# Performance work log

Hardware: AMD Instinct MI355X
Metric: run time of the kernel (lower is better)

Reference implementation:

```python
import jax, jax.numpy as jnp
import numpy as np

B, C_IN, T = 32, 22, 5000
EMB, P = 64, 100
HOP, NFFT, SR = 25, 128, 250
MIN_SZ, MAX_SZ = 10, 100
OC = 40
SCALES = (9, 25, 49)
FC = OC * len(SCALES)
_freqs = np.arange(NFFT // 2 + 1) * SR / NFFT
MU_IDX = np.nonzero((_freqs >= 8) & (_freqs <= 13))[0]   # bins 5,6
BETA_IDX = np.nonzero((_freqs >= 13) & (_freqs <= 30))[0]  # bins 7..15


def setup_inputs() -> dict:
    key = jax.random.key(0)
    k = iter(jax.random.split(key, 16))
    inp = {"x": jax.random.normal(next(k), (B, C_IN, T), jnp.float32)}
    for i, s in enumerate(SCALES):
        inp[f"ms{i}_w1"] = jax.random.normal(next(k), (OC, 1, 1, s), jnp.float32) * 0.05
        inp[f"ms{i}_b1"] = jnp.zeros((OC,), jnp.float32)
        inp[f"ms{i}_w2"] = jax.random.normal(next(k), (OC, OC, C_IN, 1), jnp.float32) * 0.05
        inp[f"ms{i}_b2"] = jnp.zeros((OC,), jnp.float32)
        inp[f"ms{i}_g"] = jnp.ones((OC,), jnp.float32)
        inp[f"ms{i}_bt"] = jnp.zeros((OC,), jnp.float32)
        inp[f"ms{i}_m"] = jnp.zeros((OC,), jnp.float32)
        inp[f"ms{i}_v"] = jnp.ones((OC,), jnp.float32)
    inp["a_w1"] = jax.random.normal(next(k), (C_IN // 2, C_IN, 3), jnp.float32) * 0.05
    inp["a_b1"] = jnp.zeros((C_IN // 2,), jnp.float32)
    inp["a_g"] = jnp.ones((C_IN // 2,), jnp.float32)
    inp["a_bt"] = jnp.zeros((C_IN // 2,), jnp.float32)
    inp["a_m"] = jnp.zeros((C_IN // 2,), jnp.float32)
    inp["a_v"] = jnp.ones((C_IN // 2,), jnp.float32)
    inp["a_w2"] = jax.random.normal(next(k), (1, C_IN // 2, 1), jnp.float32) * 0.05
    inp["a_b2"] = jnp.zeros((1,), jnp.float32)
    inp["proj_w"] = jax.random.normal(next(k), (EMB, FC, 1), jnp.float32) * 0.05
    inp["proj_b"] = jnp.zeros((EMB,), jnp.float32)
    return inp


def _conv1d(x, w, pad):
    return jax.lax.conv_general_dilated(x, w, (1,), [(pad, pad)],
                                        dimension_numbers=("NCH", "OIH", "NCH"))


def _bn(y, g, bt, m, v):  # eval-mode BatchNorm over channel dim of [B, C, T]
    return (y - m[None, :, None]) * jax.lax.rsqrt(v[None, :, None] + 1e-5) * g[None, :, None] + bt[None, :, None]


def _branch(x, w1, b1, w2, b2, g, bt, m, v):
    # Conv2d(1,OC,(1,ks)) on [B,1,C,T] == per-channel 1D conv over time.
    oc, _, _, ks = w1.shape
    b_, c_, t_ = x.shape
    y = _conv1d(x.reshape(b_ * c_, 1, t_), w1.reshape(oc, 1, ks), (ks - 1) // 2) + b1[None, :, None]
    y = y.reshape(b_, c_, oc, t_).transpose(0, 2, 1, 3)            # [B, OC, C, T]
    # Conv2d(OC,OC,(C,1)) collapses the channel (height) dim.
    y = jnp.einsum("oih,biht->bot", w2[..., 0], y) + b2[None, :, None]
    return jax.nn.elu(_bn(y, g, bt, m, v))                         # [B, OC, T]


def _stft_power(x):
    # torchaudio Spectrogram: center=True, reflect pad, periodic hann, power=2
    pad = NFFT // 2
    xp = jnp.pad(x, ((0, 0), (0, 0), (pad, pad)), mode="reflect")
    nfr = T // HOP  # module truncates to t // hop frames
    idx = jnp.arange(nfr)[:, None] * HOP + jnp.arange(NFFT)[None, :]
    win = 0.5 * (1.0 - jnp.cos(2.0 * jnp.pi * jnp.arange(NFFT) / NFFT))
    frames = xp[..., idx] * win                                    # [B, C, nfr, NFFT]
    spec = jnp.fft.rfft(frames, axis=-1)
    return spec.real ** 2 + spec.imag ** 2                         # [B, C, nfr, NFFT//2+1]


def _interp_linear(a, n):  # F.interpolate(mode='linear', align_corners=False) on [B, L]
    L = a.shape[-1]
    pos = jnp.clip((jnp.arange(n) + 0.5) * (L / n) - 0.5, 0.0, L - 1.0)
    lo = jnp.floor(pos).astype(jnp.int32)
    hi = jnp.minimum(lo + 1, L - 1)
    w = pos - lo
    return a[:, lo] * (1.0 - w) + a[:, hi] * w


def _adaptive_grid(act):
    w = 1.0 / (act + 1e-6)
    w = w / jnp.sum(w, axis=1, keepdims=True)
    gs = jnp.clip(w * T, MIN_SZ, MAX_SZ)
    gs = gs * (T / jnp.sum(gs, axis=1, keepdims=True))
    gsr = jnp.round(gs).astype(jnp.int32)
    gsr = gsr.at[:, -1].add(T - jnp.sum(gsr, axis=1))
    gsf = jnp.clip(gsr, MIN_SZ, MAX_SZ)
    gsf = gsf.at[:, -1].add(T - jnp.sum(gsf, axis=1))
    return jnp.where(gsf < MIN_SZ, MIN_SZ, gsf)


def _forward(x, ms0_w1, ms0_b1, ms0_w2, ms0_b2, ms0_g, ms0_bt, ms0_m, ms0_v,
             ms1_w1, ms1_b1, ms1_w2, ms1_b2, ms1_g, ms1_bt, ms1_m, ms1_v,
             ms2_w1, ms2_b1, ms2_w2, ms2_b2, ms2_g, ms2_bt, ms2_m, ms2_v,
             a_w1, a_b1, a_g, a_bt, a_m, a_v, a_w2, a_b2, proj_w, proj_b):
    # ---- frequency-domain activity detector ----
    spec = _stft_power(x)                                          # [B, C, 200, F]
    comb = spec[..., MU_IDX].mean(-1) + spec[..., BETA_IDX].mean(-1)  # [B, C, 200]
    a = jax.nn.relu(_bn(_conv1d(comb, a_w1, 1) + a_b1[None, :, None], a_g, a_bt, a_m, a_v))
    a = jnp.einsum("oi,bit->bot", a_w2[..., 0], a)[:, 0] + a_b2[0]
    activity = jax.nn.sigmoid(a)                                   # [B, 200]
    act_i = _interp_linear(activity, P)                            # [B, P]
    grid = _adaptive_grid(act_i)                                   # [B, P] int32, sums ~= T
    ends = jnp.cumsum(grid, axis=1)
    starts = ends - grid
    # ---- multi-scale CNN features ----
    feats = jnp.concatenate([
        _branch(x, ms0_w1, ms0_b1, ms0_w2, ms0_b2, ms0_g, ms0_bt, ms0_m, ms0_v),
        _branch(x, ms1_w1, ms1_b1, ms1_w2, ms1_b2, ms1_g, ms1_bt, ms1_m, ms1_v),
        _branch(x, ms2_w1, ms2_b1, ms2_w2, ms2_b2, ms2_g, ms2_bt, ms2_m, ms2_v)],
        axis=1)                                                    # [B, FC, T]
    # ---- ragged per-patch avg+max pooling via segment reductions ----
    tix = jnp.arange(T)
    seg = jax.vmap(lambda e: jnp.searchsorted(e, tix, side="right"))(ends)  # [B,T] in [0,P]
    flat = (seg + jnp.arange(B)[:, None] * (P + 1)).reshape(-1)
    f = feats.transpose(0, 2, 1).reshape(B * T, FC)
    nseg = B * (P + 1)  # extra slot collects any overflow timesteps
    sums = jax.ops.segment_sum(f, flat, num_segments=nseg)
    cnt = jax.ops.segment_sum(jnp.ones((B * T, 1), f.dtype), flat, num_segments=nseg)
    mx = jax.ops.segment_max(f, flat, num_segments=nseg)
    avg = sums / jnp.maximum(cnt, 1.0)
    mx = jnp.where(cnt > 0, mx, 0.0)
    pooled = (avg + mx).reshape(B, P + 1, FC)[:, :P]               # combined avg+max
    valid = ((ends <= T) & (starts < ends))[..., None]
    pooled = jnp.where(valid, pooled, 0.0)
    emb = jnp.einsum("oc,bpc->bpo", proj_w[..., 0], pooled) + proj_b  # [B, P, EMB]
    return emb, grid, act_i


def reference(x, ms0_w1, ms0_b1, ms0_w2, ms0_b2, ms0_g, ms0_bt, ms0_m, ms0_v,
              ms1_w1, ms1_b1, ms1_w2, ms1_b2, ms1_g, ms1_bt, ms1_m, ms1_v,
              ms2_w1, ms2_b1, ms2_w2, ms2_b2, ms2_g, ms2_bt, ms2_m, ms2_v,
              a_w1, a_b1, a_g, a_bt, a_m, a_v, a_w2, a_b2, proj_w, proj_b):
    return _forward(x, ms0_w1, ms0_b1, ms0_w2, ms0_b2, ms0_g, ms0_bt, ms0_m, ms0_v,
                    ms1_w1, ms1_b1, ms1_w2, ms1_b2, ms1_g, ms1_bt, ms1_m, ms1_v,
                    ms2_w1, ms2_b1, ms2_w2, ms2_b2, ms2_g, ms2_bt, ms2_m, ms2_v,
                    a_w1, a_b1, a_g, a_bt, a_m, a_v, a_w2, a_b2, proj_w, proj_b)
```

## Files before the change

kernel.cpp:

```cpp
#include <hip/hip_runtime.h>
#include <hip/hip_bf16.h>
#include <hip/hip_fp8.h>
#include <math.h>
#include <string.h>

#define B 32
#define CIN 22
#define T 5000
#define EMB 64
#define P 100
#define HOP 25
#define OC 40
#define FC 120
#define NBIN 11
#define NFR 200

#define TCH 256
#define CROWS 304
#define RS8 40

#define XPAD 5128
#define TWROW 24

typedef __attribute__((ext_vector_type(4))) float f32x4;

__device__ __forceinline__ unsigned short f2bf(float f) {
  unsigned u = __float_as_uint(f);
  unsigned r = (u + 0x7FFFu + ((u >> 16) & 1u)) >> 16;
  return (unsigned short)r;
}
__device__ __forceinline__ float bf2f(unsigned short u) {
  return __uint_as_float(((unsigned)u) << 16);
}
__device__ __forceinline__ unsigned char f2fp8(float f) {
  __hip_fp8_e4m3 q(f);
  return (unsigned char)q.__x;
}
__device__ __forceinline__ float fast_elu(float y) {
  return y > 0.f ? y : (__builtin_amdgcn_exp2f(y * 1.44269504088896340736f) - 1.0f);
}
__device__ __forceinline__ unsigned pack2bf(float a, float b) {
  __hip_bfloat162 h = __float22bfloat162_rn(make_float2(a, b));
  unsigned u;
  memcpy(&u, &h, 4);
  return u;
}
__device__ __forceinline__ float wave_sum_f(float v) {
  #pragma unroll
  for (int off = 1; off < 64; off <<= 1) v += __shfl_xor(v, off);
  return v;
}
__device__ __forceinline__ int wave_sum_i(int v) {
  #pragma unroll
  for (int off = 1; off < 64; off <<= 1) v += __shfl_xor(v, off);
  return v;
}

struct SetupArgs {
  const float* w1[3]; const float* b1[3]; const float* w2[3]; const float* b2[3];
  const float* g[3];  const float* bt[3]; const float* m[3];  const float* v[3];
  unsigned char* pw8;
  float* A; float* Bc; float* tw;
};

__global__ __launch_bounds__(256) void setup_all(SetupArgs args) {
  int bx = blockIdx.x;
  int tid = threadIdx.x;
  if (bx < 498) {
    int id = bx * 256 + tid;
    int s, KS, fbase, idl;
    if (id < 13824)       { s = 0; KS = 9;  fbase = 0;   idl = id; }
    else if (id < 52224)  { s = 1; KS = 25; fbase = 27;  idl = id - 13824; }
    else                  { s = 2; KS = 49; fbase = 102; idl = id - 52224; }
    int fi = idl >> 9, rem = idl & 511;
    int lane = rem >> 3, j = rem & 7;
    int k = fi / 3, ot = fi - k * 3;
    int m = lane & 15, h = ((lane >> 4) << 3) + j;
    int o = ot * 16 + m;
    float val = 0.f;
    if (h < CIN && o < OC) {
      const float* w1 = args.w1[s];
      const float* w2 = args.w2[s];
      for (int i = 0; i < OC; ++i)
        val = fmaf(w2[(o * OC + i) * CIN + h], w1[i * KS + k], val);
    }
    args.pw8[(size_t)(fbase + fi) * 512 + rem] = f2fp8(val);
  } else if (bx < 504) {
    int id = (bx - 498) * 256 + tid;
    if (id < 1408) {
      int n = id & 127, k = id >> 7;
      const double PI = 3.14159265358979323846;
      double ang = -2.0 * PI * (double)((k + 5) * n) / 128.0;
      double win = 0.5 * (1.0 - cos(2.0 * PI * (double)n / 128.0));
      args.tw[n * TWROW + 2 * k]     = (float)(cos(ang) * win);
      args.tw[n * TWROW + 2 * k + 1] = (float)(sin(ang) * win);
    } else if (id < 1536) {
      int n = id - 1408;
      args.tw[n * TWROW + 22] = 0.f;
      args.tw[n * TWROW + 23] = 0.f;
    }
  } else {
    if (tid < 120) {
      int s = tid / 40, o = tid - s * 40;
      const float* w2 = args.w2[s];
      float sc = args.g[s][o] / sqrtf(args.v[s][o] + 1e-5f);
      float cc = args.b2[s][o];
      for (int i = 0; i < OC; ++i) {
        float sh = 0.f;
        for (int h = 0; h < CIN; ++h) sh += w2[(o * OC + i) * CIN + h];
        cc = fmaf(args.b1[s][i], sh, cc);
      }
      args.A[tid] = sc;
      args.Bc[tid] = cc * sc + (args.bt[s][o] - args.m[s][o] * sc);
    }
  }
}

__global__ __launch_bounds__(256) void stft_comb(const float* __restrict__ x,
                                                 const float* __restrict__ tw,
                                                 float* __restrict__ comb) {
  __shared__ float xsh[XPAD];
  int bc = blockIdx.x;
  const float* xr = x + (size_t)bc * T;
  int tid = threadIdx.x;
  for (int i = tid; i < XPAD; i += 256) {
    int mm = i - 64;
    mm = (mm < 0) ? -mm : mm;
    mm = (mm >= T) ? (2 * T - 2 - mm) : mm;
    xsh[i] = xr[mm];
  }
  __syncthreads();
  int fr = tid;
  if (fr < NFR) {
    float cr[NBIN], ci[NBIN];
    #pragma unroll
    for (int k = 0; k < NBIN; ++k) { cr[k] = 0.f; ci[k] = 0.f; }
    const float* xw = xsh + fr * HOP;
    #pragma unroll 2
    for (int n = 0; n < 128; ++n) {
      float xv = xw[n];
      const float4* t4 = reinterpret_cast<const float4*>(tw + n * TWROW);
      float4 w0 = t4[0], w1 = t4[1], w2 = t4[2], w3 = t4[3], w4 = t4[4], w5 = t4[5];
      cr[0] = fmaf(xv, w0.x, cr[0]); ci[0] = fmaf(xv, w0.y, ci[0]);
      cr[1] = fmaf(xv, w0.z, cr[1]); ci[1] = fmaf(xv, w0.w, ci[1]);
      cr[2] = fmaf(xv, w1.x, cr[2]); ci[2] = fmaf(xv, w1.y, ci[2]);
      cr[3] = fmaf(xv, w1.z, cr[3]); ci[3] = fmaf(xv, w1.w, ci[3]);
      cr[4] = fmaf(xv, w2.x, cr[4]); ci[4] = fmaf(xv, w2.y, ci[4]);
      cr[5] = fmaf(xv, w2.z, cr[5]); ci[5] = fmaf(xv, w2.w, ci[5]);
      cr[6] = fmaf(xv, w3.x, cr[6]); ci[6] = fmaf(xv, w3.y, ci[6]);
      cr[7] = fmaf(xv, w3.z, cr[7]); ci[7] = fmaf(xv, w3.w, ci[7]);
      cr[8] = fmaf(xv, w4.x, cr[8]); ci[8] = fmaf(xv, w4.y, ci[8]);
      cr[9] = fmaf(xv, w4.z, cr[9]); ci[9] = fmaf(xv, w4.w, ci[9]);
      cr[10] = fmaf(xv, w5.x, cr[10]); ci[10] = fmaf(xv, w5.y, ci[10]);
    }
    float p[NBIN];
    #pragma unroll
    for (int k = 0; k < NBIN; ++k) p[k] = cr[k] * cr[k] + ci[k] * ci[k];
    float beta = 0.f;
    #pragma unroll
    for (int k = 2; k < NBIN; ++k) beta += p[k];
    comb[bc * NFR + fr] = 0.5f * (p[0] + p[1]) + beta * (1.f / 9.f);
  }
}

struct MidSmem {
  union {
    struct {
      float cl[CIN * NFR];
      float actL[NFR];
      float aiL[P];
      float fL[P];
      int giL[P];
      int sI[P];
      float red;
    } a;
    unsigned char xs8[CROWS * RS8];
  };
};

template <int KS, int FB, int SBASE>
__device__ __forceinline__ void scale_body(const unsigned char* __restrict__ xs8,
                                           const unsigned char* __restrict__ pw8,
                                           const float* __restrict__ Aff,
                                           const float* __restrict__ Bff,
                                           unsigned short* __restrict__ feats,
                                           int b, int t0, int wt0, int lane) {
  constexpr int PAD = (KS - 1) / 2;
  const int n = lane & 15, q = lane >> 4;
  f32x4 acc[3][4];
  #pragma unroll
  for (int ot = 0; ot < 3; ++ot)
    #pragma unroll
    for (int ti = 0; ti < 4; ++ti)
      acc[ot][ti] = (f32x4){0.f, 0.f, 0.f, 0.f};

  const unsigned char* pws = pw8 + (size_t)FB * 512 + lane * 8;
  long long A0 = *(const long long*)(pws);
  long long A1 = *(const long long*)(pws + 512);
  long long A2 = *(const long long*)(pws + 1024);
  #pragma unroll 1
  for (int k = 0; k < KS; ++k) {
    long long nA0 = 0, nA1 = 0, nA2 = 0;
    if (k + 1 < KS) {
      const unsigned char* p = pws + (size_t)(k + 1) * 3 * 512;
      nA0 = *(const long long*)(p);
      nA1 = *(const long long*)(p + 512);
      nA2 = *(const long long*)(p + 1024);
    }
    int rbase = 24 - PAD + k + wt0 + n;
    #pragma unroll
    for (int ti = 0; ti < 4; ++ti) {
      long long Bf = *(const long long*)(xs8 + (rbase + ti * 16) * RS8 + q * 8);
      acc[0][ti] = __builtin_amdgcn_mfma_f32_16x16x32_fp8_fp8(A0, Bf, acc[0][ti], 0, 0, 0);
      acc[1][ti] = __builtin_amdgcn_mfma_f32_16x16x32_fp8_fp8(A1, Bf, acc[1][ti], 0, 0, 0);
      acc[2][ti] = __builtin_amdgcn_mfma_f32_16x16x32_fp8_fp8(A2, Bf, acc[2][ti], 0, 0, 0);
    }
    A0 = nA0; A1 = nA1; A2 = nA2;
  }
  #pragma unroll
  for (int ot = 0; ot < 3; ++ot) {
    int obase = ot * 16 + q * 4;
    if (obase < OC) {
      float Av0 = Aff[SBASE + obase + 0], Bv0 = Bff[SBASE + obase + 0];
      float Av1 = Aff[SBASE + obase + 1], Bv1 = Bff[SBASE + obase + 1];
      float Av2 = Aff[SBASE + obase + 2], Bv2 = Bff[SBASE + obase + 2];
      float Av3 = Aff[SBASE + obase + 3], Bv3 = Bff[SBASE + obase + 3];
      #pragma unroll
      for (int ti = 0; ti < 4; ++ti) {
        int tt = t0 + wt0 + ti * 16 + n;
        if (tt < T) {
          uint2 pk;
          pk.x = pack2bf(fast_elu(fmaf(acc[ot][ti][0], Av0, Bv0)),
                         fast_elu(fmaf(acc[ot][ti][1], Av1, Bv1)));
          pk.y = pack2bf(fast_elu(fmaf(acc[ot][ti][2], Av2, Bv2)),
                         fast_elu(fmaf(acc[ot][ti][3], Av3, Bv3)));
          *reinterpret_cast<uint2*>(feats + (size_t)(b * T + tt) * FC + SBASE + obase) = pk;
        }
      }
    }
  }
}

struct MidArgs {
  const float* x;
  const unsigned char* pw8;
  const float* Aff; const float* Bff;
  unsigned short* feats;
  const float* comb;
  const float* aw1; const float* ab1;
  const float* ag;  const float* abt;
  const float* am;  const float* av;
  const float* aw2; const float* ab2;
  float* out_grid; float* out_acti;
  int* ends_i; int* grid_i;
};

__global__ __launch_bounds__(256) void mid_all(MidArgs args) {
  __shared__ MidSmem sm;
  int bx = blockIdx.x;
  int tid = threadIdx.x;
  if (bx >= B) {
    int cx = bx - B;
    int s = cx % 3;
    int rem = cx / 3;
    int b = rem / 20, t0 = (rem - b * 20) * TCH;
    for (int i = tid; i < CROWS * RS8 / 4; i += 256)
      reinterpret_cast<unsigned*>(sm.xs8)[i] = 0u;
    __syncthreads();
    for (int idx = tid; idx < CIN * CROWS; idx += 256) {
      int h = idx / CROWS, tl = idx - h * CROWS;
      int gt = t0 - 24 + tl;
      float v = (gt >= 0 && gt < T) ? args.x[(size_t)(b * CIN + h) * T + gt] : 0.f;
      sm.xs8[tl * RS8 + h] = f2fp8(v);
    }
    __syncthreads();
    int wv = tid >> 6, lane = tid & 63;
    int wt0 = wv * 64;
    if (s == 0)
      scale_body<9, 0, 0>(sm.xs8, args.pw8, args.Aff, args.Bff, args.feats, b, t0, wt0, lane);
    else if (s == 1)
      scale_body<25, 27, 40>(sm.xs8, args.pw8, args.Aff, args.Bff, args.feats, b, t0, wt0, lane);
    else
      scale_body<49, 102, 80>(sm.xs8, args.pw8, args.Aff, args.Bff, args.feats, b, t0, wt0, lane);
  } else {
    int b = bx;
    for (int i = tid; i < CIN * NFR; i += 256) sm.a.cl[i] = args.comb[b * CIN * NFR + i];
    __syncthreads();
    int t = tid;
    if (t < NFR) {
      float z = args.ab2[0];
      for (int o = 0; o < 11; ++o) {
        float s = args.ab1[o];
        for (int i = 0; i < CIN; ++i) {
          const float* wr = args.aw1 + o * 66 + i * 3;
          const float* crow = sm.a.cl + i * NFR;
          if (t > 0)       s = fmaf(wr[0], crow[t - 1], s);
          s = fmaf(wr[1], crow[t], s);
          if (t < NFR - 1) s = fmaf(wr[2], crow[t + 1], s);
        }
        float rs = 1.0f / sqrtf(args.av[o] + 1e-5f);
        float y = (s - args.am[o]) * rs * args.ag[o] + args.abt[o];
        y = fmaxf(y, 0.f);
        z = fmaf(args.aw2[o], y, z);
      }
      sm.a.actL[t] = 1.f / (1.f + expf(-z));
    }
    __syncthreads();
    if (t < P) {
      float ai = 0.5f * (sm.a.actL[2 * t] + sm.a.actL[2 * t + 1]);
      sm.a.aiL[t] = ai;
      args.out_acti[b * P + t] = ai;
      sm.a.fL[t] = 1.f / (ai + 1e-6f);
    }
    __syncthreads();
    if (t < 64) {
      float v = sm.a.fL[t] + ((t + 64 < P) ? sm.a.fL[t + 64] : 0.f);
      v = wave_sum_f(v);
      if (t == 0) sm.a.red = v;
    }
    __syncthreads();
    float sw = sm.a.red;
    if (t < P) {
      float ggv = (sm.a.fL[t] / sw) * 5000.f;
      ggv = fminf(fmaxf(ggv, 10.f), 100.f);
      sm.a.fL[t] = ggv;
    }
    __syncthreads();
    if (t < 64) {
      float v = sm.a.fL[t] + ((t + 64 < P) ? sm.a.fL[t + 64] : 0.f);
      v = wave_sum_f(v);
      if (t == 0) sm.a.red = v;
    }
    __syncthreads();
    float r = 5000.f / sm.a.red;
    if (t < P) sm.a.giL[t] = (int)rintf(sm.a.fL[t] * r);
    __syncthreads();
    if (t < 64) {
      int v = sm.a.giL[t] + ((t + 64 < P) ? sm.a.giL[t + 64] : 0);
      v = wave_sum_i(v);
      if (t == 0) sm.a.red = __int_as_float(v);
    }
    __syncthreads();
    if (t == P - 1) sm.a.giL[P - 1] += 5000 - __float_as_int(sm.a.red);
    __syncthreads();
    if (t < P) sm.a.giL[t] = min(max(sm.a.giL[t], 10), 100);
    __syncthreads();
    if (t < 64) {
      int v = sm.a.giL[t] + ((t + 64 < P) ? sm.a.giL[t + 64] : 0);
      v = wave_sum_i(v);
      if (t == 0) sm.a.red = __int_as_float(v);
    }
    __syncthreads();
    if (t == P - 1) sm.a.giL[P - 1] += 5000 - __float_as_int(sm.a.red);
    __syncthreads();
    if (t < P) sm.a.sI[t] = max(sm.a.giL[t], 10);
    __syncthreads();
    #pragma unroll
    for (int off = 1; off < P; off <<= 1) {
      int v = 0;
      if (t < P && t >= off) v = sm.a.sI[t - off];
      __syncthreads();
      if (t < P) sm.a.sI[t] += v;
      __syncthreads();
    }
    if (t < P) {
      int g2 = max(sm.a.giL[t], 10);
      args.out_grid[b * P + t] = (float)g2;
      args.grid_i[b * P + t] = g2;
      args.ends_i[b * P + t] = sm.a.sI[t];
    }
  }
}

__global__ __launch_bounds__(256) void pool_proj(const unsigned short* __restrict__ feats,
                                                 const int* __restrict__ ends_i,
                                                 const int* __restrict__ grid_i,
                                                 const float* __restrict__ proj_w,
                                                 const float* __restrict__ proj_b,
                                                 float* __restrict__ out_emb) {
  int bp = blockIdx.x;
  int b = bp / P;
  int end = ends_i[bp];
  int gr = grid_i[bp];
  int start = end - gr;
  __shared__ float lds_s[16 * FC];
  __shared__ float lds_m[16 * FC];
  __shared__ float pooled[FC];
  int tid = threadIdx.x;
  bool valid = (end <= T);
  int g = tid % 15;
  int r = tid / 15;
  if (valid && r < 16) {
    float s[8], m[8];
    #pragma unroll
    for (int j = 0; j < 8; ++j) { s[j] = 0.f; m[j] = -INFINITY; }
    const unsigned short* base = feats + (size_t)(b * T + start) * FC + g * 8;
    for (int i = r; i < gr; i += 16) {
      uint4 u4 = *reinterpret_cast<const uint4*>(base + (size_t)i * FC);
      unsigned w[4] = {u4.x, u4.y, u4.z, u4.w};
      #pragma unroll
      for (int j = 0; j < 4; ++j) {
        float v0 = bf2f((unsigned short)(w[j] & 0xffffu));
        float v1 = bf2f((unsigned short)(w[j] >> 16));
        s[2 * j] += v0; s[2 * j + 1] += v1;
        m[2 * j] = fmaxf(m[2 * j], v0); m[2 * j + 1] = fmaxf(m[2 * j + 1], v1);
      }
    }
    #pragma unroll
    for (int j = 0; j < 8; ++j) {
      lds_s[r * FC + g * 8 + j] = s[j];
      lds_m[r * FC + g * 8 + j] = m[j];
    }
  }
  __syncthreads();
  if (tid < FC) {
    if (valid) {
      float s = 0.f, mx = -INFINITY;
      #pragma unroll
      for (int rr = 0; rr < 16; ++rr) {
        s += lds_s[rr * FC + tid];
        mx = fmaxf(mx, lds_m[rr * FC + tid]);
      }
      pooled[tid] = s / (float)gr + mx;
    } else {
      pooled[tid] = 0.f;
    }
  }
  __syncthreads();
  if (tid < EMB) {
    float e = proj_b[tid];
    const float* wr = proj_w + tid * FC;
    #pragma unroll 8
    for (int c = 0; c < FC; ++c) e = fmaf(wr[c], pooled[c], e);
    out_emb[(size_t)bp * EMB + tid] = e;
  }
}

extern "C" void kernel_launch(void* const* d_in, const int* in_sizes, int n_in,
                              void* d_out, int out_size, void* d_ws, size_t ws_size,
                              hipStream_t stream) {
  const float* x = (const float*)d_in[0];
  const float* aw1 = (const float*)d_in[25];
  const float* ab1 = (const float*)d_in[26];
  const float* ag  = (const float*)d_in[27];
  const float* abt = (const float*)d_in[28];
  const float* am  = (const float*)d_in[29];
  const float* av  = (const float*)d_in[30];
  const float* aw2 = (const float*)d_in[31];
  const float* ab2 = (const float*)d_in[32];
  const float* proj_w = (const float*)d_in[33];
  const float* proj_b = (const float*)d_in[34];

  float* wsf = (float*)d_ws;
  float* A    = wsf;
  float* Bc   = wsf + 120;
  float* tw   = wsf + 240;
  float* comb = wsf + 4096;
  int* ends_i = (int*)(wsf + 144896);
  int* grid_i = (int*)(wsf + 148096);
  unsigned char* pw8 = (unsigned char*)(wsf + 151296);
  unsigned short* feats = (unsigned short*)(wsf + 215040);

  float* out      = (float*)d_out;
  float* out_emb  = out;
  float* out_grid = out + 204800;
  float* out_acti = out + 208000;

  SetupArgs sa;
  MidArgs ma;
  for (int s = 0; s < 3; ++s) {
    sa.w1[s] = (const float*)d_in[1 + 8 * s];
    sa.b1[s] = (const float*)d_in[2 + 8 * s];
    sa.w2[s] = (const float*)d_in[3 + 8 * s];
    sa.b2[s] = (const float*)d_in[4 + 8 * s];
    sa.g[s]  = (const float*)d_in[5 + 8 * s];
    sa.bt[s] = (const float*)d_in[6 + 8 * s];
    sa.m[s]  = (const float*)d_in[7 + 8 * s];
    sa.v[s]  = (const float*)d_in[8 + 8 * s];
  }
  sa.pw8 = pw8; sa.A = A; sa.Bc = Bc; sa.tw = tw;

  ma.x = x; ma.pw8 = pw8; ma.Aff = A; ma.Bff = Bc; ma.feats = feats;
  ma.comb = comb; ma.aw1 = aw1; ma.ab1 = ab1; ma.ag = ag; ma.abt = abt;
  ma.am = am; ma.av = av; ma.aw2 = aw2; ma.ab2 = ab2;
  ma.out_grid = out_grid; ma.out_acti = out_acti;
  ma.ends_i = ends_i; ma.grid_i = grid_i;

  setup_all<<<505, 256, 0, stream>>>(sa);
  stft_comb<<<B * CIN, 256, 0, stream>>>(x, tw, comb);
  mid_all<<<B + 60 * B, 256, 0, stream>>>(ma);
  pool_proj<<<B * P, 256, 0, stream>>>(feats, ends_i, grid_i, proj_w, proj_b, out_emb);
}
```

Baseline: 270.2 us.

## Fuse three conv scales per block and vectorize fp8 weight folding

```diff
diff --git a/kernel.cpp b/kernel.cpp
--- a/kernel.cpp
+++ b/kernel.cpp
@@ -66,27 +66,59 @@
 __global__ __launch_bounds__(256) void setup_all(SetupArgs args) {
   int bx = blockIdx.x;
   int tid = threadIdx.x;
-  if (bx < 498) {
+  if (bx < 63) {
     int id = bx * 256 + tid;
-    int s, KS, fbase, idl;
-    if (id < 13824)       { s = 0; KS = 9;  fbase = 0;   idl = id; }
-    else if (id < 52224)  { s = 1; KS = 25; fbase = 27;  idl = id - 13824; }
-    else                  { s = 2; KS = 49; fbase = 102; idl = id - 52224; }
-    int fi = idl >> 9, rem = idl & 511;
-    int lane = rem >> 3, j = rem & 7;
-    int k = fi / 3, ot = fi - k * 3;
-    int m = lane & 15, h = ((lane >> 4) << 3) + j;
-    int o = ot * 16 + m;
-    float val = 0.f;
-    if (h < CIN && o < OC) {
-      const float* w1 = args.w1[s];
-      const float* w2 = args.w2[s];
-      for (int i = 0; i < OC; ++i)
-        val = fmaf(w2[(o * OC + i) * CIN + h], w1[i * KS + k], val);
-    }
-    args.pw8[(size_t)(fbase + fi) * 512 + rem] = f2fp8(val);
-  } else if (bx < 504) {
-    int id = (bx - 498) * 256 + tid;
+    if (id < 15936) {
+      int fi = id >> 6;
+      int lane = id & 63;
+      int s, KS, fl;
+      if (fi < 27)       { s = 0; KS = 9;  fl = fi; }
+      else if (fi < 102) { s = 1; KS = 25; fl = fi - 27; }
+      else               { s = 2; KS = 49; fl = fi - 102; }
+      int k = fl / 3, ot = fl - k * 3;
+      int m = lane & 15, hb = (lane >> 4) << 3;
+      int o = ot * 16 + m;
+      float val[8];
+      #pragma unroll
+      for (int j = 0; j < 8; ++j) val[j] = 0.f;
+      if (o < OC && hb < CIN) {
+        const float* w1 = args.w1[s];
+        const float* w2 = args.w2[s];
+        if (hb + 8 <= CIN) {
+          for (int i = 0; i < OC; ++i) {
+            float wv = w1[i * KS + k];
+            const float* w2r = w2 + (size_t)(o * OC + i) * CIN + hb;
+            float2 a0 = *(const float2*)(w2r + 0);
+            float2 a1 = *(const float2*)(w2r + 2);
+            float2 a2 = *(const float2*)(w2r + 4);
+            float2 a3 = *(const float2*)(w2r + 6);
+            val[0] = fmaf(a0.x, wv, val[0]); val[1] = fmaf(a0.y, wv, val[1]);
+            val[2] = fmaf(a1.x, wv, val[2]); val[3] = fmaf(a1.y, wv, val[3]);
+            val[4] = fmaf(a2.x, wv, val[4]); val[5] = fmaf(a2.y, wv, val[5]);
+            val[6] = fmaf(a3.x, wv, val[6]); val[7] = fmaf(a3.y, wv, val[7]);
+          }
+        } else {
+          for (int i = 0; i < OC; ++i) {
+            float wv = w1[i * KS + k];
+            const float* w2r = w2 + (size_t)(o * OC + i) * CIN + hb;
+            float2 a0 = *(const float2*)(w2r + 0);
+            float2 a1 = *(const float2*)(w2r + 2);
+            float2 a2 = *(const float2*)(w2r + 4);
+            val[0] = fmaf(a0.x, wv, val[0]); val[1] = fmaf(a0.y, wv, val[1]);
+            val[2] = fmaf(a1.x, wv, val[2]); val[3] = fmaf(a1.y, wv, val[3]);
+            val[4] = fmaf(a2.x, wv, val[4]); val[5] = fmaf(a2.y, wv, val[5]);
+          }
+        }
+      }
+      unsigned char bytes[8];
+      #pragma unroll
+      for (int j = 0; j < 8; ++j) bytes[j] = f2fp8(val[j]);
+      long long pk;
+      memcpy(&pk, bytes, 8);
+      *(long long*)(args.pw8 + (size_t)fi * 512 + lane * 8) = pk;
+    }
+  } else if (bx < 69) {
+    int id = (bx - 63) * 256 + tid;
     if (id < 1408) {
       int n = id & 127, k = id >> 7;
       const double PI = 3.14159265358979323846;
@@ -187,11 +219,11 @@
                                            int b, int t0, int wt0, int lane) {
   constexpr int PAD = (KS - 1) / 2;
   const int n = lane & 15, q = lane >> 4;
-  f32x4 acc[3][4];
+  f32x4 acc[3][2];
   #pragma unroll
   for (int ot = 0; ot < 3; ++ot)
     #pragma unroll
-    for (int ti = 0; ti < 4; ++ti)
+    for (int ti = 0; ti < 2; ++ti)
       acc[ot][ti] = (f32x4){0.f, 0.f, 0.f, 0.f};
 
   const unsigned char* pws = pw8 + (size_t)FB * 512 + lane * 8;
@@ -209,7 +241,7 @@
     }
     int rbase = 24 - PAD + k + wt0 + n;
     #pragma unroll
-    for (int ti = 0; ti < 4; ++ti) {
+    for (int ti = 0; ti < 2; ++ti) {
       long long Bf = *(const long long*)(xs8 + (rbase + ti * 16) * RS8 + q * 8);
       acc[0][ti] = __builtin_amdgcn_mfma_f32_16x16x32_fp8_fp8(A0, Bf, acc[0][ti], 0, 0, 0);
       acc[1][ti] = __builtin_amdgcn_mfma_f32_16x16x32_fp8_fp8(A1, Bf, acc[1][ti], 0, 0, 0);
@@ -226,7 +258,7 @@
       float Av2 = Aff[SBASE + obase + 2], Bv2 = Bff[SBASE + obase + 2];
       float Av3 = Aff[SBASE + obase + 3], Bv3 = Bff[SBASE + obase + 3];
       #pragma unroll
-      for (int ti = 0; ti < 4; ++ti) {
+      for (int ti = 0; ti < 2; ++ti) {
         int tt = t0 + wt0 + ti * 16 + n;
         if (tt < T) {
           uint2 pk;
@@ -255,19 +287,17 @@
   int* ends_i; int* grid_i;
 };
 
-__global__ __launch_bounds__(256) void mid_all(MidArgs args) {
+__global__ __launch_bounds__(512) void mid_all(MidArgs args) {
   __shared__ MidSmem sm;
   int bx = blockIdx.x;
   int tid = threadIdx.x;
   if (bx >= B) {
     int cx = bx - B;
-    int s = cx % 3;
-    int rem = cx / 3;
-    int b = rem / 20, t0 = (rem - b * 20) * TCH;
-    for (int i = tid; i < CROWS * RS8 / 4; i += 256)
+    int b = cx / 20, t0 = (cx - b * 20) * TCH;
+    for (int i = tid; i < CROWS * RS8 / 4; i += 512)
       reinterpret_cast<unsigned*>(sm.xs8)[i] = 0u;
     __syncthreads();
-    for (int idx = tid; idx < CIN * CROWS; idx += 256) {
+    for (int idx = tid; idx < CIN * CROWS; idx += 512) {
       int h = idx / CROWS, tl = idx - h * CROWS;
       int gt = t0 - 24 + tl;
       float v = (gt >= 0 && gt < T) ? args.x[(size_t)(b * CIN + h) * T + gt] : 0.f;
@@ -275,16 +305,13 @@
     }
     __syncthreads();
     int wv = tid >> 6, lane = tid & 63;
-    int wt0 = wv * 64;
-    if (s == 0)
-      scale_body<9, 0, 0>(sm.xs8, args.pw8, args.Aff, args.Bff, args.feats, b, t0, wt0, lane);
-    else if (s == 1)
-      scale_body<25, 27, 40>(sm.xs8, args.pw8, args.Aff, args.Bff, args.feats, b, t0, wt0, lane);
-    else
-      scale_body<49, 102, 80>(sm.xs8, args.pw8, args.Aff, args.Bff, args.feats, b, t0, wt0, lane);
+    int wt0 = wv * 32;
+    scale_body<9, 0, 0>(sm.xs8, args.pw8, args.Aff, args.Bff, args.feats, b, t0, wt0, lane);
+    scale_body<25, 27, 40>(sm.xs8, args.pw8, args.Aff, args.Bff, args.feats, b, t0, wt0, lane);
+    scale_body<49, 102, 80>(sm.xs8, args.pw8, args.Aff, args.Bff, args.feats, b, t0, wt0, lane);
   } else {
     int b = bx;
-    for (int i = tid; i < CIN * NFR; i += 256) sm.a.cl[i] = args.comb[b * CIN * NFR + i];
+    for (int i = tid; i < CIN * NFR; i += 512) sm.a.cl[i] = args.comb[b * CIN * NFR + i];
     __syncthreads();
     int t = tid;
     if (t < NFR) {
@@ -486,8 +513,8 @@
   ma.out_grid = out_grid; ma.out_acti = out_acti;
   ma.ends_i = ends_i; ma.grid_i = grid_i;
 
-  setup_all<<<505, 256, 0, stream>>>(sa);
+  setup_all<<<70, 256, 0, stream>>>(sa);
   stft_comb<<<B * CIN, 256, 0, stream>>>(x, tw, comb);
-  mid_all<<<B + 60 * B, 256, 0, stream>>>(ma);
+  mid_all<<<B + 20 * B, 512, 0, stream>>>(ma);
   pool_proj<<<B * P, 256, 0, stream>>>(feats, ends_i, grid_i, proj_w, proj_b, out_emb);
 }
```

New measurement: 262.8 us. 1.03x faster.
